# Kernel tuning notes

Hardware: AMD Instinct MI355X
Metric: run time of the kernel (lower is better)

Reference implementation:

```python
import jax, jax.numpy as jnp
import numpy as np

K = 128
NITER = 10


def _sq_dist(x, c):
    x2 = jnp.sum(x * x, axis=1, keepdims=True)          # [N,1]
    c2 = jnp.sum(c * c, axis=1)                          # [K]
    return x2 + c2[None, :] - 2.0 * (x @ c.T)


def _kmeans(x, key):
    N, D = x.shape
    idx = jax.random.permutation(key, N)[:K]             # torch.randperm(N)[:K]
    c0 = x[idx]

    def step(c, _):
        cl = jnp.argmin(_sq_dist(x, c), axis=1)          # nearest assignment [N]
        counts = jax.ops.segment_sum(jnp.ones((N,), x.dtype), cl, num_segments=K)  # bincount
        sums = jax.ops.segment_sum(x, cl, num_segments=K)                          # [K,D] (vectorized over D)
        # c = sums / counts; NaN (empty cluster, 0/0) -> 0, matching c[isnan(c)]=0
        c_new = jnp.where(counts[:, None] > 0, sums / jnp.maximum(counts, 1.0)[:, None], 0.0)
        return c_new, None

    c, _ = jax.lax.scan(step, c0, None, length=NITER)
    return c


def setup_inputs() -> dict:
    key = jax.random.key(0)
    x = jax.random.normal(key, (500000, 64), dtype=jnp.float32)
    return {"x": x}


def reference(x):
    # KMeans runs on x.detach(); forward output has no grad path through centroids
    centroids = _kmeans(jax.lax.stop_gradient(x), jax.random.key(42))
    distances = _sq_dist(x, centroids)                   # [N, K]
    # Faithful to normalize_distance: distances.sum(1, keepdim=True)[0] indexes
    # ROW 0 of the [N,1] row-sums -> a single scalar broadcast to all rows.
    denom = jnp.sum(distances[0])
    probs = 1.0 - distances / denom
    return probs
```

## Files before the change

### kernel.cpp

```cpp
#include <hip/hip_runtime.h>
#include <cstdint>
#include <cstddef>

#define NPTS 500000
#define DIM 64
#define KC 128
#define KM_ITERS 10
#define NGROUPS (NPTS / 32)
#define NITERS8 ((NGROUPS + 7) / 8)

typedef __bf16 bf16x8 __attribute__((ext_vector_type(8)));
typedef float f32x4 __attribute__((ext_vector_type(4)));

__device__ __forceinline__ float wave_reduce_add(float v) {
#pragma unroll
  for (int off = 32; off > 0; off >>= 1) v += __shfl_xor(v, off, 64);
  return v;
}

__device__ __forceinline__ bf16x8 cvt8(float4 a, float4 b) {
  bf16x8 r;
  r[0] = (__bf16)a.x; r[1] = (__bf16)a.y; r[2] = (__bf16)a.z; r[3] = (__bf16)a.w;
  r[4] = (__bf16)b.x; r[5] = (__bf16)b.y; r[6] = (__bf16)b.z; r[7] = (__bf16)b.w;
  return r;
}

__global__ void k_initc(const float* __restrict__ x, float* __restrict__ cent,
                        float* __restrict__ c2, float* __restrict__ sums,
                        float* __restrict__ cnts) {
  int k = blockIdx.x, d = threadIdx.x;
  long src = (long)k * 3891 + 7;
  float v = x[src * DIM + d];
  cent[k * DIM + d] = v;
  sums[k * DIM + d] = 0.f;
  float s = wave_reduce_add(v * v);
  if (d == 0) { c2[k] = s; cnts[k] = 0.f; }
}

__global__ void k_update(const float* __restrict__ sums, const float* __restrict__ cnts,
                         float* __restrict__ cent, float* __restrict__ c2,
                         float* __restrict__ sums_z, float* __restrict__ cnts_z) {
  int k = blockIdx.x, d = threadIdx.x;
  float c = cnts[k];
  float v = (c > 0.f) ? (sums[k * DIM + d] / c) : 0.f;
  cent[k * DIM + d] = v;
  sums_z[k * DIM + d] = 0.f;
  float s = wave_reduce_add(v * v);
  if (d == 0) { c2[k] = s; cnts_z[k] = 0.f; }
}

#define DIST_H(V0, V1, MK)                                                     \
  {                                                                            \
    f32x4 acc_[8];                                                             \
    _Pragma("unroll") for (int tt = 0; tt < 8; tt++)                           \
      acc_[tt] = (f32x4){c2h[tt * 4 + 0], c2h[tt * 4 + 1],                     \
                         c2h[tt * 4 + 2], c2h[tt * 4 + 3]};                    \
    _Pragma("unroll") for (int tt = 0; tt < 8; tt++)                           \
      acc_[tt] = __builtin_amdgcn_mfma_f32_16x16x32_bf16(afr0[tt], V0, acc_[tt], 0, 0, 0); \
    _Pragma("unroll") for (int tt = 0; tt < 8; tt++)                           \
      acc_[tt] = __builtin_amdgcn_mfma_f32_16x16x32_bf16(afr1[tt], V1, acc_[tt], 0, 0, 0); \
    float tv[32]; int ti[32];                                                  \
    _Pragma("unroll") for (int i_ = 0; i_ < 32; i_++) {                        \
      tv[i_] = acc_[i_ >> 2][i_ & 3]; ti[i_] = i_;                             \
    }                                                                          \
    _Pragma("unroll") for (int s_ = 16; s_ >= 1; s_ >>= 1)                     \
      _Pragma("unroll") for (int i_ = 0; i_ < s_; i_++) {                      \
        bool t_ = tv[i_ + s_] > tv[i_];                                        \
        tv[i_] = t_ ? tv[i_ + s_] : tv[i_];                                    \
        ti[i_] = t_ ? ti[i_ + s_] : ti[i_];                                    \
      }                                                                        \
    float maxv = tv[0];                                                        \
    int mk = ((ti[0] >> 2) << 4) + grp * 4 + (ti[0] & 3);                      \
    _Pragma("unroll") for (int off = 16; off <= 32; off <<= 1) {               \
      float ov = __shfl_xor(maxv, off, 64);                                    \
      int ok = __shfl_xor(mk, off, 64);                                        \
      if (ov > maxv || (ov == maxv && ok < mk)) { maxv = ov; mk = ok; }        \
    }                                                                          \
    MK = mk;                                                                   \
  }

#define XT_WRITE(XTW, V0, V1, H)                                               \
  {                                                                            \
    int slotb = (((((H) << 1) | (col >> 3)) ^ grp) & 3) * 16 + (col & 7) * 2;  \
    _Pragma("unroll") for (int j = 0; j < 8; j++) {                            \
      *(__bf16*)((XTW) + (grp * 8 + j) * 80 + slotb) = V0[j];                  \
      *(__bf16*)((XTW) + (32 + grp * 8 + j) * 80 + slotb) = V1[j];             \
    }                                                                          \
  }

template <int FIRST>
__global__ __launch_bounds__(256, 2)
void k_assign(const float* __restrict__ xf, const __bf16* __restrict__ xb,
              __bf16* __restrict__ xbw, const float* __restrict__ cent,
              const float* __restrict__ c2, float* __restrict__ sums,
              float* __restrict__ cnts) {
  __shared__ char xT[8][5120];
  __shared__ int sm[8][32];
  __shared__ float lc[KC];

  const int lane = threadIdx.x & 63;
  const int wid = threadIdx.x >> 6;
  const int col = lane & 15;
  const int grp = lane >> 4;

  bf16x8 afr0[8], afr1[8];
  float c2h[32];
#pragma unroll
  for (int t = 0; t < 8; t++) {
    const float* cp = cent + (size_t)(t * 16 + col) * DIM;
    afr0[t] = cvt8(*(const float4*)(cp + grp * 8), *(const float4*)(cp + grp * 8 + 4));
    afr1[t] = cvt8(*(const float4*)(cp + 32 + grp * 8), *(const float4*)(cp + 32 + grp * 8 + 4));
#pragma unroll
    for (int r = 0; r < 4; r++) c2h[t * 4 + r] = -0.5f * c2[t * 16 + grp * 4 + r];
  }
#pragma unroll
  for (int t = 0; t < 8; t++) asm volatile("" : "+v"(afr0[t]), "+v"(afr1[t]));
#pragma unroll
  for (int i = 0; i < 32; i++) asm volatile("" : "+v"(c2h[i]));

  for (int i = threadIdx.x; i < KC; i += 256) lc[i] = 0.f;
  __syncthreads();

  f32x4 accs[8];
#pragma unroll
  for (int i = 0; i < 8; i++) accs[i] = (f32x4){0.f, 0.f, 0.f, 0.f};

  const int kbase = wid * 32;

  bf16x8 p0a, p1a, p0b, p1b;
  if constexpr (!FIRST) {
    int g0 = blockIdx.x * 8 + wid * 2;
    if (blockIdx.x < NITERS8 && g0 < NGROUPS) {
      const bf16x8* xr = (const bf16x8*)(xb + (size_t)(g0 * 32 + col) * DIM + grp * 8);
      p0a = xr[0]; p1a = xr[4]; p0b = xr[128]; p1b = xr[132];
    }
  }

  for (int it = blockIdx.x; it < NITERS8; it += gridDim.x) {
    int g0 = it * 8 + wid * 2, g1 = g0 + 1;
    bool e0 = g0 < NGROUPS, e1 = g1 < NGROUPS;

    bf16x8 v0a, v1a, v0b, v1b, w0a, w1a, w0b, w1b;
    if constexpr (FIRST) {
      if (e0) {
        const float* xp = xf + (size_t)(g0 * 32 + col) * DIM + grp * 8;
        const float* xq = xp + 16 * DIM;
        v0a = cvt8(*(const float4*)xp, *(const float4*)(xp + 4));
        v1a = cvt8(*(const float4*)(xp + 32), *(const float4*)(xp + 36));
        v0b = cvt8(*(const float4*)xq, *(const float4*)(xq + 4));
        v1b = cvt8(*(const float4*)(xq + 32), *(const float4*)(xq + 36));
        bf16x8* wp = (bf16x8*)(xbw + (size_t)(g0 * 32 + col) * DIM);
        wp[grp] = v0a; wp[4 + grp] = v1a; wp[128 + grp] = v0b; wp[132 + grp] = v1b;
      }
      if (e1) {
        const float* xp = xf + (size_t)(g1 * 32 + col) * DIM + grp * 8;
        const float* xq = xp + 16 * DIM;
        w0a = cvt8(*(const float4*)xp, *(const float4*)(xp + 4));
        w1a = cvt8(*(const float4*)(xp + 32), *(const float4*)(xp + 36));
        w0b = cvt8(*(const float4*)xq, *(const float4*)(xq + 4));
        w1b = cvt8(*(const float4*)(xq + 32), *(const float4*)(xq + 36));
        bf16x8* wp = (bf16x8*)(xbw + (size_t)(g1 * 32 + col) * DIM);
        wp[grp] = w0a; wp[4 + grp] = w1a; wp[128 + grp] = w0b; wp[132 + grp] = w1b;
      }
    } else {
      v0a = p0a; v1a = p1a; v0b = p0b; v1b = p1b;
      if (e1) {
        const bf16x8* xr = (const bf16x8*)(xb + (size_t)(g1 * 32 + col) * DIM + grp * 8);
        w0a = xr[0]; w1a = xr[4]; w0b = xr[128]; w1b = xr[132];
      }
    }

    int mk0a = -1, mk0b = -1, mk1a = -1, mk1b = -1;
    if (e0) {
      char* xTw = xT[wid * 2];
      XT_WRITE(xTw, v0a, v1a, 0);
      XT_WRITE(xTw, v0b, v1b, 1);
      DIST_H(v0a, v1a, mk0a);
      DIST_H(v0b, v1b, mk0b);
      if (grp == 0) { atomicAdd(&lc[mk0a], 1.f); atomicAdd(&lc[mk0b], 1.f); }
    }
    if (grp == 0) { sm[wid * 2][col] = mk0a; sm[wid * 2][16 + col] = mk0b; }
    if (e1) {
      char* xTw = xT[wid * 2 + 1];
      XT_WRITE(xTw, w0a, w1a, 0);
      XT_WRITE(xTw, w0b, w1b, 1);
      DIST_H(w0a, w1a, mk1a);
      DIST_H(w0b, w1b, mk1b);
      if (grp == 0) { atomicAdd(&lc[mk1a], 1.f); atomicAdd(&lc[mk1b], 1.f); }
    }
    if (grp == 0) { sm[wid * 2 + 1][col] = mk1a; sm[wid * 2 + 1][16 + col] = mk1b; }
    __syncthreads();

    if constexpr (!FIRST) {
      int itn = it + gridDim.x;
      int g0n = itn * 8 + wid * 2;
      if (itn < NITERS8 && g0n < NGROUPS) {
        const bf16x8* xr = (const bf16x8*)(xb + (size_t)(g0n * 32 + col) * DIM + grp * 8);
        p0a = xr[0]; p1a = xr[4]; p0b = xr[128]; p1b = xr[132];
      }
    }

#pragma unroll
    for (int G = 0; G < 8; G++) {
      const int* smG = sm[G];
      int4 mlo = *(const int4*)&smG[grp * 8];
      int4 mhi = *(const int4*)&smG[grp * 8 + 4];
      const char* xTg = xT[G];
      bf16x8 xf0, xf1, xf2, xf3;
      { int d = col;      int s = (grp ^ ((d >> 3) & 3)) & 3; xf0 = *(const bf16x8*)(xTg + d * 80 + s * 16); }
      { int d = 16 + col; int s = (grp ^ ((d >> 3) & 3)) & 3; xf1 = *(const bf16x8*)(xTg + d * 80 + s * 16); }
      { int d = 32 + col; int s = (grp ^ ((d >> 3) & 3)) & 3; xf2 = *(const bf16x8*)(xTg + d * 80 + s * 16); }
      { int d = 48 + col; int s = (grp ^ ((d >> 3) & 3)) & 3; xf3 = *(const bf16x8*)(xTg + d * 80 + s * 16); }
      int m0 = mlo.x, m1 = mlo.y, m2 = mlo.z, m3 = mlo.w;
      int m4 = mhi.x, m5 = mhi.y, m6 = mhi.z, m7 = mhi.w;
#pragma unroll
      for (int tt2 = 0; tt2 < 2; tt2++) {
        int c = kbase + tt2 * 16 + col;
        union { unsigned u[4]; bf16x8 v; } oh;
        oh.u[0] = (m0 == c ? 0x3F80u : 0u) | (m1 == c ? 0x3F800000u : 0u);
        oh.u[1] = (m2 == c ? 0x3F80u : 0u) | (m3 == c ? 0x3F800000u : 0u);
        oh.u[2] = (m4 == c ? 0x3F80u : 0u) | (m5 == c ? 0x3F800000u : 0u);
        oh.u[3] = (m6 == c ? 0x3F80u : 0u) | (m7 == c ? 0x3F800000u : 0u);
        accs[tt2 * 4 + 0] = __builtin_amdgcn_mfma_f32_16x16x32_bf16(oh.v, xf0, accs[tt2 * 4 + 0], 0, 0, 0);
        accs[tt2 * 4 + 1] = __builtin_amdgcn_mfma_f32_16x16x32_bf16(oh.v, xf1, accs[tt2 * 4 + 1], 0, 0, 0);
        accs[tt2 * 4 + 2] = __builtin_amdgcn_mfma_f32_16x16x32_bf16(oh.v, xf2, accs[tt2 * 4 + 2], 0, 0, 0);
        accs[tt2 * 4 + 3] = __builtin_amdgcn_mfma_f32_16x16x32_bf16(oh.v, xf3, accs[tt2 * 4 + 3], 0, 0, 0);
      }
    }
    __syncthreads();
  }

#pragma unroll
  for (int tt2 = 0; tt2 < 2; tt2++)
#pragma unroll
    for (int dt = 0; dt < 4; dt++)
#pragma unroll
      for (int r = 0; r < 4; r++)
        atomicAdd(&sums[(size_t)(kbase + tt2 * 16 + grp * 4 + r) * DIM + dt * 16 + col],
                  accs[tt2 * 4 + dt][r]);
  for (int i = threadIdx.x; i < KC; i += 256) atomicAdd(&cnts[i], lc[i]);
}

__global__ __launch_bounds__(256, 2)
void k_probs(const float* __restrict__ x, const float* __restrict__ cent,
             const float* __restrict__ c2, float* __restrict__ out) {
  const int lane = threadIdx.x & 63;
  const int wid = threadIdx.x >> 6;
  const int col = lane & 15;
  const int grp = lane >> 4;

  bf16x8 afr[2][8];
  float c2g[32];
#pragma unroll
  for (int t = 0; t < 8; t++) {
    const float* cp = cent + (size_t)(t * 16 + col) * DIM;
#pragma unroll
    for (int ks = 0; ks < 2; ks++) {
      float4 f0 = *(const float4*)(cp + ks * 32 + grp * 8);
      float4 f1 = *(const float4*)(cp + ks * 32 + grp * 8 + 4);
      afr[ks][t] = cvt8(f0, f1);
    }
#pragma unroll
    for (int r = 0; r < 4; r++) c2g[t * 4 + r] = c2[t * 16 + grp * 4 + r];
  }

  float c2a = c2[lane], c2b = c2[64 + lane];
  float x2_0 = 0.f, dA = 0.f, dB = 0.f;
#pragma unroll 8
  for (int d = 0; d < DIM; d++) {
    float xv = x[d];
    x2_0 = fmaf(xv, xv, x2_0);
    dA = fmaf(xv, cent[(size_t)lane * DIM + d], dA);
    dB = fmaf(xv, cent[(size_t)(64 + lane) * DIM + d], dB);
  }
  float part = ((x2_0 + c2a) - 2.f * dA) + ((x2_0 + c2b) - 2.f * dB);
  float invd = 1.0f / wave_reduce_add(part);

  int w = blockIdx.x * 4 + wid;
  int nw = gridDim.x * 4;
  for (int t = w; t < NPTS / 16; t += nw) {
    int n0 = t * 16;
    const float* xp = x + (size_t)(n0 + col) * DIM;
    float4 a0 = *(const float4*)(xp + grp * 8);
    float4 a1 = *(const float4*)(xp + grp * 8 + 4);
    float4 b0 = *(const float4*)(xp + 32 + grp * 8);
    float4 b1 = *(const float4*)(xp + 32 + grp * 8 + 4);
    bf16x8 xb0 = cvt8(a0, a1), xb1 = cvt8(b0, b1);

    float sq = a0.x * a0.x + a0.y * a0.y + a0.z * a0.z + a0.w * a0.w
             + a1.x * a1.x + a1.y * a1.y + a1.z * a1.z + a1.w * a1.w
             + b0.x * b0.x + b0.y * b0.y + b0.z * b0.z + b0.w * b0.w
             + b1.x * b1.x + b1.y * b1.y + b1.z * b1.z + b1.w * b1.w;
    sq += __shfl_xor(sq, 16, 64);
    sq += __shfl_xor(sq, 32, 64);

    f32x4 acc[8];
#pragma unroll
    for (int tt = 0; tt < 8; tt++) acc[tt] = (f32x4){0.f, 0.f, 0.f, 0.f};
#pragma unroll
    for (int tt = 0; tt < 8; tt++)
      acc[tt] = __builtin_amdgcn_mfma_f32_16x16x32_bf16(afr[0][tt], xb0, acc[tt], 0, 0, 0);
#pragma unroll
    for (int tt = 0; tt < 8; tt++)
      acc[tt] = __builtin_amdgcn_mfma_f32_16x16x32_bf16(afr[1][tt], xb1, acc[tt], 0, 0, 0);

    float* op = out + (size_t)(n0 + col) * KC + grp * 4;
#pragma unroll
    for (int tt = 0; tt < 8; tt++) {
      f32x4 q;
      q[0] = 1.f - ((sq + c2g[tt * 4 + 0]) - 2.f * acc[tt][0]) * invd;
      q[1] = 1.f - ((sq + c2g[tt * 4 + 1]) - 2.f * acc[tt][1]) * invd;
      q[2] = 1.f - ((sq + c2g[tt * 4 + 2]) - 2.f * acc[tt][2]) * invd;
      q[3] = 1.f - ((sq + c2g[tt * 4 + 3]) - 2.f * acc[tt][3]) * invd;
      __builtin_nontemporal_store(q, (f32x4*)(op + tt * 16));
    }
  }
}

extern "C" void kernel_launch(void* const* d_in, const int* in_sizes, int n_in,
                              void* d_out, int out_size, void* d_ws, size_t ws_size,
                              hipStream_t stream) {
  const float* x = (const float*)d_in[0];
  float* out = (float*)d_out;

  float* cent = (float*)d_ws;
  float* c2 = cent + KC * DIM;
  float* sums = c2 + KC;
  float* cnts = sums + KC * DIM;

  __bf16* xb = (__bf16*)d_out;

  k_initc<<<KC, DIM, 0, stream>>>(x, cent, c2, sums, cnts);
  k_assign<1><<<512, 256, 0, stream>>>(x, xb, xb, cent, c2, sums, cnts);
  k_update<<<KC, DIM, 0, stream>>>(sums, cnts, cent, c2, sums, cnts);
  for (int it = 1; it < KM_ITERS; it++) {
    k_assign<0><<<512, 256, 0, stream>>>(x, xb, xb, cent, c2, sums, cnts);
    k_update<<<KC, DIM, 0, stream>>>(sums, cnts, cent, c2, sums, cnts);
  }
  k_probs<<<512, 256, 0, stream>>>(x, cent, c2, out);
}
```

Measured before the change: 675.0 us.

## Fold centroid update into assign kernel using per-iteration sum buffers

Removes the separate k_update launch between k-means iterations. Each k_assign now rebuilds the centroids itself from the previous iteration's sums and counts, including their squared norms. To make that possible without a zeroing pass, every iteration gets its own sums/counts buffer, all cleared once in k_initc. This saves nine small kernel launches and their serialization, at the cost of every block redundantly reading the 32KB sums buffer and doing a reciprocal/normalization prologue.

New measurement: 666.9 us. No clear change (-1.2%).

```diff
diff --git a/kernel.cpp b/kernel.cpp
--- a/kernel.cpp
+++ b/kernel.cpp
@@ -26,27 +26,27 @@
 }
 
 __global__ void k_initc(const float* __restrict__ x, float* __restrict__ cent,
-                        float* __restrict__ c2, float* __restrict__ sums,
-                        float* __restrict__ cnts) {
+                        float* __restrict__ c2, float* __restrict__ S,
+                        float* __restrict__ CNT) {
   int k = blockIdx.x, d = threadIdx.x;
   long src = (long)k * 3891 + 7;
   float v = x[src * DIM + d];
   cent[k * DIM + d] = v;
-  sums[k * DIM + d] = 0.f;
+#pragma unroll
+  for (int p = 0; p < KM_ITERS; p++) S[p * (KC * DIM) + k * DIM + d] = 0.f;
+  if (d < KM_ITERS) CNT[d * KC + k] = 0.f;
   float s = wave_reduce_add(v * v);
-  if (d == 0) { c2[k] = s; cnts[k] = 0.f; }
+  if (d == 0) c2[k] = s;
 }
 
 __global__ void k_update(const float* __restrict__ sums, const float* __restrict__ cnts,
-                         float* __restrict__ cent, float* __restrict__ c2,
-                         float* __restrict__ sums_z, float* __restrict__ cnts_z) {
+                         float* __restrict__ cent, float* __restrict__ c2) {
   int k = blockIdx.x, d = threadIdx.x;
   float c = cnts[k];
   float v = (c > 0.f) ? (sums[k * DIM + d] / c) : 0.f;
   cent[k * DIM + d] = v;
-  sums_z[k * DIM + d] = 0.f;
   float s = wave_reduce_add(v * v);
-  if (d == 0) { c2[k] = s; cnts_z[k] = 0.f; }
+  if (d == 0) c2[k] = s;
 }
 
 #define DIST_H(V0, V1, MK)                                                     \
@@ -88,15 +88,24 @@
     }                                                                          \
   }
 
+#define SSQ16(F0, F1, G0, G1)                                                  \
+  ((F0.x * F0.x + F0.y * F0.y + F0.z * F0.z + F0.w * F0.w) +                   \
+   (F1.x * F1.x + F1.y * F1.y + F1.z * F1.z + F1.w * F1.w) +                   \
+   (G0.x * G0.x + G0.y * G0.y + G0.z * G0.z + G0.w * G0.w) +                   \
+   (G1.x * G1.x + G1.y * G1.y + G1.z * G1.z + G1.w * G1.w))
+
 template <int FIRST>
 __global__ __launch_bounds__(256, 2)
 void k_assign(const float* __restrict__ xf, const __bf16* __restrict__ xb,
               __bf16* __restrict__ xbw, const float* __restrict__ cent,
-              const float* __restrict__ c2, float* __restrict__ sums,
-              float* __restrict__ cnts) {
+              const float* __restrict__ c2, const float* __restrict__ s_prev,
+              const float* __restrict__ cnt_prev, float* __restrict__ s_out,
+              float* __restrict__ cnt_out) {
   __shared__ char xT[8][5120];
   __shared__ int sm[8][32];
   __shared__ float lc[KC];
+  __shared__ float lcnt[KC];
+  __shared__ float lc2[KC];
 
   const int lane = threadIdx.x & 63;
   const int wid = threadIdx.x >> 6;
@@ -105,21 +114,57 @@
 
   bf16x8 afr0[8], afr1[8];
   float c2h[32];
-#pragma unroll
-  for (int t = 0; t < 8; t++) {
-    const float* cp = cent + (size_t)(t * 16 + col) * DIM;
-    afr0[t] = cvt8(*(const float4*)(cp + grp * 8), *(const float4*)(cp + grp * 8 + 4));
-    afr1[t] = cvt8(*(const float4*)(cp + 32 + grp * 8), *(const float4*)(cp + 32 + grp * 8 + 4));
-#pragma unroll
-    for (int r = 0; r < 4; r++) c2h[t * 4 + r] = -0.5f * c2[t * 16 + grp * 4 + r];
+
+  if constexpr (FIRST) {
+    for (int i = threadIdx.x; i < KC; i += 256) lc[i] = 0.f;
+#pragma unroll
+    for (int t = 0; t < 8; t++) {
+      const float* cp = cent + (size_t)(t * 16 + col) * DIM;
+      afr0[t] = cvt8(*(const float4*)(cp + grp * 8), *(const float4*)(cp + grp * 8 + 4));
+      afr1[t] = cvt8(*(const float4*)(cp + 32 + grp * 8), *(const float4*)(cp + 32 + grp * 8 + 4));
+#pragma unroll
+      for (int r = 0; r < 4; r++) c2h[t * 4 + r] = -0.5f * c2[t * 16 + grp * 4 + r];
+    }
+    __syncthreads();
+  } else {
+    for (int i = threadIdx.x; i < KC; i += 256) { lcnt[i] = cnt_prev[i]; lc[i] = 0.f; }
+    __syncthreads();
+    float ssq[8];
+#pragma unroll
+    for (int t = 0; t < 8; t++) {
+      int row = t * 16 + col;
+      float c = lcnt[row];
+      float inv = (c > 0.f) ? 1.f / c : 0.f;
+      const float* sp = s_prev + (size_t)row * DIM;
+      float4 f0 = *(const float4*)(sp + grp * 8);
+      float4 f1 = *(const float4*)(sp + grp * 8 + 4);
+      float4 g0 = *(const float4*)(sp + 32 + grp * 8);
+      float4 g1 = *(const float4*)(sp + 32 + grp * 8 + 4);
+      f0.x *= inv; f0.y *= inv; f0.z *= inv; f0.w *= inv;
+      f1.x *= inv; f1.y *= inv; f1.z *= inv; f1.w *= inv;
+      g0.x *= inv; g0.y *= inv; g0.z *= inv; g0.w *= inv;
+      g1.x *= inv; g1.y *= inv; g1.z *= inv; g1.w *= inv;
+      afr0[t] = cvt8(f0, f1);
+      afr1[t] = cvt8(g0, g1);
+      ssq[t] = SSQ16(f0, f1, g0, g1);
+    }
+#pragma unroll
+    for (int t = 0; t < 8; t++) {
+      float s = ssq[t];
+      s += __shfl_xor(s, 16, 64);
+      s += __shfl_xor(s, 32, 64);
+      if (lane < 16 && wid == 0) lc2[t * 16 + col] = s;
+    }
+    __syncthreads();
+#pragma unroll
+    for (int t = 0; t < 8; t++)
+#pragma unroll
+      for (int r = 0; r < 4; r++) c2h[t * 4 + r] = -0.5f * lc2[t * 16 + grp * 4 + r];
   }
 #pragma unroll
   for (int t = 0; t < 8; t++) asm volatile("" : "+v"(afr0[t]), "+v"(afr1[t]));
 #pragma unroll
   for (int i = 0; i < 32; i++) asm volatile("" : "+v"(c2h[i]));
-
-  for (int i = threadIdx.x; i < KC; i += 256) lc[i] = 0.f;
-  __syncthreads();
 
   f32x4 accs[8];
 #pragma unroll
@@ -236,9 +281,9 @@
     for (int dt = 0; dt < 4; dt++)
 #pragma unroll
       for (int r = 0; r < 4; r++)
-        atomicAdd(&sums[(size_t)(kbase + tt2 * 16 + grp * 4 + r) * DIM + dt * 16 + col],
+        atomicAdd(&s_out[(size_t)(kbase + tt2 * 16 + grp * 4 + r) * DIM + dt * 16 + col],
                   accs[tt2 * 4 + dt][r]);
-  for (int i = threadIdx.x; i < KC; i += 256) atomicAdd(&cnts[i], lc[i]);
+  for (int i = threadIdx.x; i < KC; i += 256) atomicAdd(&cnt_out[i], lc[i]);
 }
 
 __global__ __launch_bounds__(256, 2)
@@ -325,17 +370,18 @@
 
   float* cent = (float*)d_ws;
   float* c2 = cent + KC * DIM;
-  float* sums = c2 + KC;
-  float* cnts = sums + KC * DIM;
+  float* S = c2 + KC;
+  float* CNT = S + KM_ITERS * KC * DIM;
 
   __bf16* xb = (__bf16*)d_out;
 
-  k_initc<<<KC, DIM, 0, stream>>>(x, cent, c2, sums, cnts);
-  k_assign<1><<<512, 256, 0, stream>>>(x, xb, xb, cent, c2, sums, cnts);
-  k_update<<<KC, DIM, 0, stream>>>(sums, cnts, cent, c2, sums, cnts);
+  k_initc<<<KC, DIM, 0, stream>>>(x, cent, c2, S, CNT);
+  k_assign<1><<<512, 256, 0, stream>>>(x, xb, xb, cent, c2, nullptr, nullptr, S, CNT);
   for (int it = 1; it < KM_ITERS; it++) {
-    k_assign<0><<<512, 256, 0, stream>>>(x, xb, xb, cent, c2, sums, cnts);
-    k_update<<<KC, DIM, 0, stream>>>(sums, cnts, cent, c2, sums, cnts);
-  }
+    k_assign<0><<<512, 256, 0, stream>>>(x, xb, xb, cent, c2,
+                                         S + (it - 1) * KC * DIM, CNT + (it - 1) * KC,
+                                         S + it * KC * DIM, CNT + it * KC);
+  }
+  k_update<<<KC, DIM, 0, stream>>>(S + 9 * KC * DIM, CNT + 9 * KC, cent, c2);
   k_probs<<<512, 256, 0, stream>>>(x, cent, c2, out);
 }
```
